# Kernel tuning notes

Measured on AMD Instinct MI355X. Metric: run time of the kernel, lower is better.

## Reference

```python
import jax, jax.numpy as jnp
import numpy as np

E = 8          # n_experts
K = 5          # n_active = int(0.7*E)
TEMP = float(np.e)

def _l2norm(v):
    n = jnp.linalg.norm(v, axis=-1, keepdims=True)
    return v / jnp.maximum(n, 1e-12)

def setup_inputs() -> dict:
    key = jax.random.key(0)
    ks = jax.random.split(key, 13)
    N, D, H, O = 4096, 2048, 4096, 2048
    s = lambda fan: 1.0 / np.sqrt(fan)
    return {
        "x":    jax.random.normal(ks[0], (N, D), jnp.float32),
        "Wg":   jax.random.normal(ks[1], (D, E), jnp.float32) * s(D),
        "bg":   jnp.zeros((E,), jnp.float32),
        "Wa":   jax.random.normal(ks[2], (D, 32), jnp.float32) * s(D),
        "ba":   jnp.zeros((32,), jnp.float32),
        "Wb":   jax.random.normal(ks[3], (32, 16), jnp.float32) * s(32),
        "bb":   jnp.zeros((16,), jnp.float32),
        "sigs": jax.random.normal(ks[4], (E, 16), jnp.float32) * 0.1,
        "W1":   jax.random.normal(ks[5], (E, D, H), jnp.float32) * s(D),
        "b1":   jnp.zeros((E, H), jnp.float32),
        "W2":   jax.random.normal(ks[6], (E, H, O), jnp.float32) * s(H),
        "b2":   jnp.zeros((E, O), jnp.float32),
    }

def reference(x, Wg, bg, Wa, ba, Wb, bb, sigs, W1, b1, W2, b2):
    # gating softmax (temperature = e)
    probs = jax.nn.softmax((x @ Wg + bg) / TEMP, axis=-1)          # [N, E]
    # PH feature match
    ph = jax.nn.relu(x @ Wa + ba) @ Wb + bb                        # [N, 16]
    ph_match = (_l2norm(ph) @ _l2norm(sigs).T + 1.0) / 2.0         # [N, E]
    effective = probs * ph_match                                   # [N, E]
    # top-k mask over experts
    _, idx = jax.lax.top_k(effective, K)                           # [N, K]
    mask = jnp.sum(jax.nn.one_hot(idx, E, dtype=effective.dtype), axis=-2)  # [N, E]
    weights = effective * mask
    weights = weights / (weights.sum(axis=-1, keepdims=True) + 1e-8)
    # dense all-expert FFN (eval mode: dropout is identity)
    h = jax.nn.relu(jnp.einsum('nd,edh->neh', x, W1) + b1)         # [N, E, H]
    outs = jnp.einsum('neh,eho->neo', h, W2) + b2                  # [N, E, O]
    return jnp.einsum('ne,neo->no', weights, outs)                 # [N, O]
```

## Files before the change

kernel.cpp:

```cpp
#include <hip/hip_runtime.h>
#include <hip/hip_bf16.h>
#include <stdint.h>

#define TOK  4096
#define DIM  2048
#define HID  4096
#define ODIM 2048
#define NEXP 8
#define KSEL 5
#define NSLOT (TOK * KSEL)

typedef __bf16 bf16x8 __attribute__((ext_vector_type(8)));
typedef float  f32x4  __attribute__((ext_vector_type(4)));
typedef unsigned short ushort8 __attribute__((ext_vector_type(8)));

__device__ __forceinline__ uint16_t f2bf(float f) {
  uint32_t u = __float_as_uint(f);
  u += 0x7FFFu + ((u >> 16) & 1u);
  return (uint16_t)(u >> 16);
}
__device__ __forceinline__ float bf2f(uint16_t h) {
  uint32_t u = ((uint32_t)h) << 16;
  return __uint_as_float(u);
}

#define GLD16(g, l) __builtin_amdgcn_global_load_lds(                      \
    (const __attribute__((address_space(1))) void*)(g),                    \
    (__attribute__((address_space(3))) void*)(l), 16, 0, 0)


__global__ void cast_x_kernel(const float* __restrict__ in,
                              uint16_t* __restrict__ out, int n4) {
  int i = blockIdx.x * blockDim.x + threadIdx.x;
  if (i >= n4) return;
  float4 v = ((const float4*)in)[i];
  ushort4 o;
  o.x = f2bf(v.x); o.y = f2bf(v.y); o.z = f2bf(v.z); o.w = f2bf(v.w);
  ((ushort4*)out)[i] = o;
}

__global__ void transpose_cast_kernel(const float* __restrict__ in,
                                      uint16_t* __restrict__ out,
                                      int R, int C, long inBatch, long outBatch) {
  __shared__ float tile[32][33];
  const float* src = in + (size_t)blockIdx.z * inBatch;
  uint16_t*    dst = out + (size_t)blockIdx.z * outBatch;
  int c0 = blockIdx.x * 32, r0 = blockIdx.y * 32;
  int tx = threadIdx.x, ty = threadIdx.y;
#pragma unroll
  for (int i = 0; i < 4; ++i)
    tile[ty + i * 8][tx] = src[(size_t)(r0 + ty + i * 8) * C + c0 + tx];
  __syncthreads();
#pragma unroll
  for (int i = 0; i < 4; ++i)
    dst[(size_t)(c0 + ty + i * 8) * R + r0 + tx] = f2bf(tile[tx][ty + i * 8]);
}


__global__ void routing_kernel(const float* __restrict__ x,
                               const float* __restrict__ Wg, const float* __restrict__ bg,
                               const float* __restrict__ Wa, const float* __restrict__ ba,
                               const float* __restrict__ Wb, const float* __restrict__ bb,
                               const float* __restrict__ sigs,
                               float* __restrict__ wts, int* __restrict__ selmask_g) {
  const int n    = blockIdx.x;
  const int lane = threadIdx.x;
  const float* xr = x + (size_t)n * DIM;

  float ga[NEXP]; float aa[32];
#pragma unroll
  for (int e = 0; e < NEXP; ++e) ga[e] = 0.f;
#pragma unroll
  for (int j = 0; j < 32; ++j) aa[j] = 0.f;

  for (int it = 0; it < DIM / 64; ++it) {
    int d = it * 64 + lane;
    float xv = xr[d];
    const float* wgr = Wg + (size_t)d * NEXP;
#pragma unroll
    for (int e = 0; e < NEXP; ++e) ga[e] += xv * wgr[e];
    const float* war = Wa + (size_t)d * 32;
#pragma unroll
    for (int j = 0; j < 32; ++j) aa[j] += xv * war[j];
  }
#pragma unroll
  for (int s = 1; s < 64; s <<= 1) {
#pragma unroll
    for (int e = 0; e < NEXP; ++e) ga[e] += __shfl_xor(ga[e], s);
#pragma unroll
    for (int j = 0; j < 32; ++j) aa[j] += __shfl_xor(aa[j], s);
  }

  float ph[16];
#pragma unroll
  for (int i = 0; i < 16; ++i) ph[i] = bb[i];
#pragma unroll
  for (int j = 0; j < 32; ++j) {
    float a = aa[j] + ba[j];
    a = a > 0.f ? a : 0.f;
#pragma unroll
    for (int i = 0; i < 16; ++i) ph[i] += a * Wb[j * 16 + i];
  }
  float nrm = 0.f;
#pragma unroll
  for (int i = 0; i < 16; ++i) nrm += ph[i] * ph[i];
  nrm = fmaxf(sqrtf(nrm), 1e-12f);

  const float invT = 0.36787944117144233f;
  float lg[NEXP], mx = -1e30f;
#pragma unroll
  for (int e = 0; e < NEXP; ++e) { lg[e] = (ga[e] + bg[e]) * invT; mx = fmaxf(mx, lg[e]); }
  float psum = 0.f, pr[NEXP];
#pragma unroll
  for (int e = 0; e < NEXP; ++e) { pr[e] = expf(lg[e] - mx); psum += pr[e]; }

  float eff[NEXP];
#pragma unroll
  for (int e = 0; e < NEXP; ++e) {
    const float* sg = sigs + e * 16;
    float dot = 0.f, sn = 0.f;
#pragma unroll
    for (int i = 0; i < 16; ++i) { dot += ph[i] * sg[i]; sn += sg[i] * sg[i]; }
    sn = fmaxf(sqrtf(sn), 1e-12f);
    float match = (dot / (nrm * sn) + 1.f) * 0.5f;
    eff[e] = (pr[e] / psum) * match;
  }

  int selmask = 0;
#pragma unroll
  for (int t = 0; t < KSEL; ++t) {
    int bi = 0; float bv = -1e30f;
#pragma unroll
    for (int e = 0; e < NEXP; ++e) {
      bool ok = !((selmask >> e) & 1);
      if (ok && eff[e] > bv) { bv = eff[e]; bi = e; }
    }
    selmask |= (1 << bi);
  }
  float wsum = 0.f, wv[NEXP];
#pragma unroll
  for (int e = 0; e < NEXP; ++e) {
    wv[e] = ((selmask >> e) & 1) ? eff[e] : 0.f;
    wsum += wv[e];
  }
  float inv = 1.f / (wsum + 1e-8f);
  if (lane == 0) {
#pragma unroll
    for (int e = 0; e < NEXP; ++e) wts[n * NEXP + e] = wv[e] * inv;
    selmask_g[n] = selmask;
  }
}


__global__ void listbuild_kernel(const int* __restrict__ selmask_g,
                                 const float* __restrict__ wts,
                                 int* __restrict__ cnt, int* __restrict__ base,
                                 int* __restrict__ list, int* __restrict__ slot_map,
                                 float* __restrict__ wrow) {
  const int e = blockIdx.x;
  const int t = threadIdx.x;
  __shared__ int cntT[256][NEXP];
  __shared__ int totAll[NEXP];
  __shared__ int sc[256];

  int msk[16];
  int c8[NEXP];
#pragma unroll
  for (int f = 0; f < NEXP; ++f) c8[f] = 0;
#pragma unroll
  for (int i = 0; i < 16; ++i) {
    msk[i] = selmask_g[t * 16 + i];
#pragma unroll
    for (int f = 0; f < NEXP; ++f) c8[f] += (msk[i] >> f) & 1;
  }
#pragma unroll
  for (int f = 0; f < NEXP; ++f) cntT[t][f] = c8[f];
  __syncthreads();

  if (t < NEXP) {
    int s = 0;
    for (int j = 0; j < 256; ++j) s += cntT[j][t];
    totAll[t] = s;
  }
  __syncthreads();

  if (e == 0 && t == 0) {
    int r = 0;
    for (int f = 0; f < NEXP; ++f) { cnt[f] = totAll[f]; base[f] = r; r += totAll[f]; }
  }
  int gbase = 0;
  for (int f = 0; f < e; ++f) gbase += totAll[f];

  sc[t] = c8[e];
  __syncthreads();
  for (int off = 1; off < 256; off <<= 1) {
    int v = (t >= off) ? sc[t - off] : 0;
    __syncthreads();
    sc[t] += v;
    __syncthreads();
  }
  int p = sc[t] - c8[e];

#pragma unroll
  for (int i = 0; i < 16; ++i) {
    const int n = t * 16 + i;
    const int m = msk[i];
    if ((m >> e) & 1) {
      list[e * TOK + p] = n;
      const int rank = __popc(m & ((1 << e) - 1));
      slot_map[n * KSEL + rank] = gbase + p;
      wrow[gbase + p] = wts[n * NEXP + e];
      ++p;
    }
  }
}


__global__ void gemm1_kernel(const uint16_t* __restrict__ xbf,
                             const uint16_t* __restrict__ W1T,
                             const int* __restrict__ cnt,
                             const int* __restrict__ base,
                             const int* __restrict__ list,
                             const float* __restrict__ wrow,
                             const float* __restrict__ b1,
                             uint16_t* __restrict__ hbuf) {
  __shared__ __attribute__((aligned(16))) uint16_t smA[128 * 64];
  __shared__ __attribute__((aligned(16))) uint16_t smB[128 * 64];
  const int e  = blockIdx.z;
  const int ce = cnt[e];
  const int tileM = blockIdx.y * 128;
  if (tileM >= ce) return;
  const int be    = base[e];
  const int tileN = blockIdx.x * 128;
  const int tid = threadIdx.x, lane = tid & 63, wid = tid >> 6;
  const int wr = wid >> 1, wc = wid & 1;
  const int* liste = list + e * TOK;

  const uint16_t* srcA[4]; const uint16_t* srcB[4]; uint32_t lof[4];
#pragma unroll
  for (int j = 0; j < 4; ++j) {
    const int f   = (wid * 4 + j) * 64 + lane;
    const int row = f >> 3;
    const int s8  = (f & 7) ^ (row & 7);
    int p = tileM + row; p = p < ce ? p : ce - 1;
    srcA[j] = xbf + (size_t)liste[p] * DIM + s8 * 8;
    srcB[j] = W1T + ((size_t)e * HID + tileN + row) * DIM + s8 * 8;
    lof[j]  = (wid * 4 + j) * 1024;
  }

  f32x4 acc[4][4];
#pragma unroll
  for (int m = 0; m < 4; ++m)
#pragma unroll
    for (int n = 0; n < 4; ++n) acc[m][n] = (f32x4){0.f, 0.f, 0.f, 0.f};

  for (int k0 = 0; k0 < DIM; k0 += 64) {
#pragma unroll
    for (int j = 0; j < 4; ++j) {
      GLD16(srcA[j] + k0, (char*)smA + lof[j]);
      GLD16(srcB[j] + k0, (char*)smB + lof[j]);
    }
    __syncthreads();
#pragma unroll
    for (int kk = 0; kk < 2; ++kk) {
      bf16x8 av[4], bv[4];
#pragma unroll
      for (int m = 0; m < 4; ++m) {
        const int row = wr * 64 + m * 16 + (lane & 15);
        const int g   = (kk * 4 + (lane >> 4)) ^ (row & 7);
        av[m] = *(const bf16x8*)(smA + row * 64 + g * 8);
      }
#pragma unroll
      for (int n = 0; n < 4; ++n) {
        const int row = wc * 64 + n * 16 + (lane & 15);
        const int g   = (kk * 4 + (lane >> 4)) ^ (row & 7);
        bv[n] = *(const bf16x8*)(smB + row * 64 + g * 8);
      }
#pragma unroll
      for (int m = 0; m < 4; ++m)
#pragma unroll
        for (int n = 0; n < 4; ++n)
          acc[m][n] = __builtin_amdgcn_mfma_f32_16x16x32_bf16(av[m], bv[n], acc[m][n], 0, 0, 0);
    }
    __syncthreads();
  }

  const float* b1e = b1 + (size_t)e * HID;
#pragma unroll
  for (int m = 0; m < 4; ++m)
#pragma unroll
    for (int r = 0; r < 4; ++r) {
      const int p = tileM + wr * 64 + m * 16 + ((lane >> 4) << 2) + r;
      if (p < ce) {
        const float w = wrow[be + p];
        uint16_t* orow = hbuf + (size_t)(be + p) * HID;
#pragma unroll
        for (int nf = 0; nf < 4; ++nf) {
          const int col = tileN + wc * 64 + nf * 16 + (lane & 15);
          float v = acc[m][nf][r] + b1e[col];
          v = v > 0.f ? v : 0.f;
          orow[col] = f2bf(v * w);
        }
      }
    }
}


__global__ void gemm2_kernel(const uint16_t* __restrict__ hbuf,
                             const uint16_t* __restrict__ W2T,
                             const int* __restrict__ cnt,
                             const int* __restrict__ base,
                             uint16_t* __restrict__ obuf) {
  __shared__ __attribute__((aligned(16))) uint16_t smA[128 * 64];
  __shared__ __attribute__((aligned(16))) uint16_t smB[128 * 64];
  const int e  = blockIdx.z;
  const int ce = cnt[e];
  const int tileM = blockIdx.y * 128;
  if (tileM >= ce) return;
  const int be    = base[e];
  const int tileN = blockIdx.x * 128;
  const int tid = threadIdx.x, lane = tid & 63, wid = tid >> 6;
  const int wr = wid >> 1, wc = wid & 1;

  const uint16_t* srcA[4]; const uint16_t* srcB[4]; uint32_t lof[4];
#pragma unroll
  for (int j = 0; j < 4; ++j) {
    const int f   = (wid * 4 + j) * 64 + lane;
    const int row = f >> 3;
    const int s8  = (f & 7) ^ (row & 7);
    srcA[j] = hbuf + (size_t)(be + tileM + row) * HID + s8 * 8;
    srcB[j] = W2T + (size_t)(tileN + row) * (NEXP * HID) + e * HID + s8 * 8;
    lof[j]  = (wid * 4 + j) * 1024;
  }

  f32x4 acc[4][4];
#pragma unroll
  for (int m = 0; m < 4; ++m)
#pragma unroll
    for (int n = 0; n < 4; ++n) acc[m][n] = (f32x4){0.f, 0.f, 0.f, 0.f};

  for (int k0 = 0; k0 < HID; k0 += 64) {
#pragma unroll
    for (int j = 0; j < 4; ++j) {
      GLD16(srcA[j] + k0, (char*)smA + lof[j]);
      GLD16(srcB[j] + k0, (char*)smB + lof[j]);
    }
    __syncthreads();
#pragma unroll
    for (int kk = 0; kk < 2; ++kk) {
      bf16x8 av[4], bv[4];
#pragma unroll
      for (int m = 0; m < 4; ++m) {
        const int row = wr * 64 + m * 16 + (lane & 15);
        const int g   = (kk * 4 + (lane >> 4)) ^ (row & 7);
        av[m] = *(const bf16x8*)(smA + row * 64 + g * 8);
      }
#pragma unroll
      for (int n = 0; n < 4; ++n) {
        const int row = wc * 64 + n * 16 + (lane & 15);
        const int g   = (kk * 4 + (lane >> 4)) ^ (row & 7);
        bv[n] = *(const bf16x8*)(smB + row * 64 + g * 8);
      }
#pragma unroll
      for (int m = 0; m < 4; ++m)
#pragma unroll
        for (int n = 0; n < 4; ++n)
          acc[m][n] = __builtin_amdgcn_mfma_f32_16x16x32_bf16(av[m], bv[n], acc[m][n], 0, 0, 0);
    }
    __syncthreads();
  }

#pragma unroll
  for (int m = 0; m < 4; ++m)
#pragma unroll
    for (int r = 0; r < 4; ++r) {
      const int p = tileM + wr * 64 + m * 16 + ((lane >> 4) << 2) + r;
      if (p < ce) {
        uint16_t* orow = obuf + (size_t)(be + p) * ODIM;
#pragma unroll
        for (int nf = 0; nf < 4; ++nf) {
          const int col = tileN + wc * 64 + nf * 16 + (lane & 15);
          orow[col] = f2bf(acc[m][nf][r]);
        }
      }
    }
}


__global__ void reduce_kernel(const uint16_t* __restrict__ obuf,
                              const int* __restrict__ slot_map,
                              const float* __restrict__ wts,
                              const float* __restrict__ b2,
                              float* __restrict__ out) {
  const int n = blockIdx.x;
  const int t = threadIdx.x;
  const int c = t * 8;

  int slots[KSEL];
#pragma unroll
  for (int k = 0; k < KSEL; ++k) slots[k] = slot_map[n * KSEL + k];
  float w8[NEXP];
#pragma unroll
  for (int e = 0; e < NEXP; ++e) w8[e] = wts[n * NEXP + e];

  float s[8];
#pragma unroll
  for (int j = 0; j < 8; ++j) s[j] = 0.f;
#pragma unroll
  for (int e = 0; e < NEXP; ++e) {
    const float4 b0 = *(const float4*)(b2 + (size_t)e * ODIM + c);
    const float4 b1v = *(const float4*)(b2 + (size_t)e * ODIM + c + 4);
    s[0] += w8[e] * b0.x; s[1] += w8[e] * b0.y; s[2] += w8[e] * b0.z; s[3] += w8[e] * b0.w;
    s[4] += w8[e] * b1v.x; s[5] += w8[e] * b1v.y; s[6] += w8[e] * b1v.z; s[7] += w8[e] * b1v.w;
  }
#pragma unroll
  for (int k = 0; k < KSEL; ++k) {
    const ushort8 v = *(const ushort8*)(obuf + (size_t)slots[k] * ODIM + c);
#pragma unroll
    for (int j = 0; j < 8; ++j) s[j] += bf2f(v[j]);
  }
  float4 o0 = make_float4(s[0], s[1], s[2], s[3]);
  float4 o1 = make_float4(s[4], s[5], s[6], s[7]);
  *(float4*)(out + (size_t)n * ODIM + c) = o0;
  *(float4*)(out + (size_t)n * ODIM + c + 4) = o1;
}


extern "C" void kernel_launch(void* const* d_in, const int* in_sizes, int n_in,
                              void* d_out, int out_size, void* d_ws, size_t ws_size,
                              hipStream_t stream) {
  const float* x    = (const float*)d_in[0];
  const float* Wg   = (const float*)d_in[1];
  const float* bg   = (const float*)d_in[2];
  const float* Wa   = (const float*)d_in[3];
  const float* ba   = (const float*)d_in[4];
  const float* Wb   = (const float*)d_in[5];
  const float* bb   = (const float*)d_in[6];
  const float* sigs = (const float*)d_in[7];
  const float* W1   = (const float*)d_in[8];
  const float* b1   = (const float*)d_in[9];
  const float* W2   = (const float*)d_in[10];
  const float* b2   = (const float*)d_in[11];
  float* out = (float*)d_out;

  char* ws = (char*)d_ws;
  float*    wts     = (float*)(ws + 0);
  int*      selmask = (int*)(ws + 131072);
  int*      cnt     = (int*)(ws + 147456);
  int*      base    = (int*)(ws + 147584);
  int*      slot_map= (int*)(ws + 151552);
  float*    wrow    = (float*)(ws + 233472);
  int*      list    = (int*)(ws + 315392);
  uint16_t* xbf     = (uint16_t*)(ws + 446464);
  uint16_t* W1T     = (uint16_t*)(ws + 17223680);
  uint16_t* W2T     = (uint16_t*)(ws + 151441408);
  uint16_t* hbuf    = (uint16_t*)(ws + 285659136);
  uint16_t* obuf    = (uint16_t*)(ws + 453431296);

  cast_x_kernel<<<(TOK * DIM / 4) / 256, 256, 0, stream>>>(x, xbf, TOK * DIM / 4);
  transpose_cast_kernel<<<dim3(HID / 32, DIM / 32, NEXP), dim3(32, 8), 0, stream>>>(
      W1, W1T, DIM, HID, (long)DIM * HID, (long)DIM * HID);
  transpose_cast_kernel<<<dim3(ODIM / 32, (NEXP * HID) / 32, 1), dim3(32, 8), 0, stream>>>(
      W2, W2T, NEXP * HID, ODIM, 0, 0);
  routing_kernel<<<TOK, 64, 0, stream>>>(x, Wg, bg, Wa, ba, Wb, bb, sigs, wts, selmask);
  listbuild_kernel<<<NEXP, 256, 0, stream>>>(selmask, wts, cnt, base, list, slot_map, wrow);

  gemm1_kernel<<<dim3(HID / 128, TOK / 128, NEXP), 256, 0, stream>>>(
      xbf, W1T, cnt, base, list, wrow, b1, hbuf);
  gemm2_kernel<<<dim3(ODIM / 128, TOK / 128, NEXP), 256, 0, stream>>>(
      hbuf, W2T, cnt, base, obuf);
  reduce_kernel<<<TOK, 256, 0, stream>>>(obuf, slot_map, wts, b2, out);
}
```

Before: 1.766 ms.

## Remap GEMM grids to 1D with expert-interleaved grouped tile order, per-expert W2T layout

Both grouped GEMMs now use a flattened 1D grid. The expert index is the fastest-varying dimension so consecutive workgroups spread across experts, and M/N tiles are grouped (8 M-tiles per N sweep in gemm1, 4 N-tiles per M sweep in gemm2) to improve L2 reuse of the A and B tiles. W2 is now transposed per expert into an [E, ODIM, HID] layout, so each expert's B rows are contiguous instead of strided by NEXP*HID. This aims to cut cache misses and DRAM traffic. The risk is that early-exiting empty tiles now sit interleaved across the dispatch order.

```diff
diff --git a/kernel.cpp b/kernel.cpp
--- a/kernel.cpp
+++ b/kernel.cpp
@@ -8,7 +8,6 @@
 #define ODIM 2048
 #define NEXP 8
 #define KSEL 5
-#define NSLOT (TOK * KSEL)
 
 typedef __bf16 bf16x8 __attribute__((ext_vector_type(8)));
 typedef float  f32x4  __attribute__((ext_vector_type(4)));
@@ -226,12 +225,19 @@
                              uint16_t* __restrict__ hbuf) {
   __shared__ __attribute__((aligned(16))) uint16_t smA[128 * 64];
   __shared__ __attribute__((aligned(16))) uint16_t smB[128 * 64];
-  const int e  = blockIdx.z;
+  const int d = blockIdx.x;
+  const int e = d & 7;
+  const int q = d >> 3;
+  const int grp = q >> 8;
+  const int rem = q & 255;
+  const int nt  = rem >> 3;
+  const int mt  = (grp << 3) | (rem & 7);
+
   const int ce = cnt[e];
-  const int tileM = blockIdx.y * 128;
+  const int tileM = mt * 128;
   if (tileM >= ce) return;
   const int be    = base[e];
-  const int tileN = blockIdx.x * 128;
+  const int tileN = nt * 128;
   const int tid = threadIdx.x, lane = tid & 63, wid = tid >> 6;
   const int wr = wid >> 1, wc = wid & 1;
   const int* liste = list + e * TOK;
@@ -313,12 +319,19 @@
                              uint16_t* __restrict__ obuf) {
   __shared__ __attribute__((aligned(16))) uint16_t smA[128 * 64];
   __shared__ __attribute__((aligned(16))) uint16_t smB[128 * 64];
-  const int e  = blockIdx.z;
+  const int d = blockIdx.x;
+  const int e = d & 7;
+  const int q = d >> 3;
+  const int grp = q >> 7;
+  const int rem = q & 127;
+  const int mt  = rem >> 2;
+  const int nt  = (grp << 2) | (rem & 3);
+
   const int ce = cnt[e];
-  const int tileM = blockIdx.y * 128;
+  const int tileM = mt * 128;
   if (tileM >= ce) return;
   const int be    = base[e];
-  const int tileN = blockIdx.x * 128;
+  const int tileN = nt * 128;
   const int tid = threadIdx.x, lane = tid & 63, wid = tid >> 6;
   const int wr = wid >> 1, wc = wid & 1;
 
@@ -329,7 +342,7 @@
     const int row = f >> 3;
     const int s8  = (f & 7) ^ (row & 7);
     srcA[j] = hbuf + (size_t)(be + tileM + row) * HID + s8 * 8;
-    srcB[j] = W2T + (size_t)(tileN + row) * (NEXP * HID) + e * HID + s8 * 8;
+    srcB[j] = W2T + ((size_t)e * ODIM + tileN + row) * HID + s8 * 8;
     lof[j]  = (wid * 4 + j) * 1024;
   }
 
@@ -460,14 +473,14 @@
   cast_x_kernel<<<(TOK * DIM / 4) / 256, 256, 0, stream>>>(x, xbf, TOK * DIM / 4);
   transpose_cast_kernel<<<dim3(HID / 32, DIM / 32, NEXP), dim3(32, 8), 0, stream>>>(
       W1, W1T, DIM, HID, (long)DIM * HID, (long)DIM * HID);
-  transpose_cast_kernel<<<dim3(ODIM / 32, (NEXP * HID) / 32, 1), dim3(32, 8), 0, stream>>>(
-      W2, W2T, NEXP * HID, ODIM, 0, 0);
+  transpose_cast_kernel<<<dim3(ODIM / 32, HID / 32, NEXP), dim3(32, 8), 0, stream>>>(
+      W2, W2T, HID, ODIM, (long)HID * ODIM, (long)ODIM * HID);
   routing_kernel<<<TOK, 64, 0, stream>>>(x, Wg, bg, Wa, ba, Wb, bb, sigs, wts, selmask);
   listbuild_kernel<<<NEXP, 256, 0, stream>>>(selmask, wts, cnt, base, list, slot_map, wrow);
 
-  gemm1_kernel<<<dim3(HID / 128, TOK / 128, NEXP), 256, 0, stream>>>(
+  gemm1_kernel<<<NEXP * 32 * 32, 256, 0, stream>>>(
       xbf, W1T, cnt, base, list, wrow, b1, hbuf);
-  gemm2_kernel<<<dim3(ODIM / 128, TOK / 128, NEXP), 256, 0, stream>>>(
+  gemm2_kernel<<<NEXP * 32 * 16, 256, 0, stream>>>(
       hbuf, W2T, cnt, base, obuf);
   reduce_kernel<<<TOK, 256, 0, stream>>>(obuf, slot_map, wts, b2, out);
 }
```

Measured after the change: 2.173 ms. +23.0%, slower.

## Replace both expert GEMMs with a 256x256 tile, 4-stage pipelined LDS kernel

Applied to the files above, without the earlier changes.

Both expert GEMMs now share one templated kernel that uses 256x256 output tiles with 512 threads and a 4-slot LDS ring buffer (K-step 32). Global-to-LDS loads are issued three stages ahead, with explicit vmcnt waits, split barriers and setprio around the MFMA bursts, so loads overlap with compute. The W2 transpose is also changed to a per-expert layout so both GEMMs index B the same way. The larger tiles improve operand reuse, but they add register pressure (128 accumulator floats per thread) and waste more work on partial M tiles at expert-count boundaries. The LDS layout also drops the XOR swizzle, which risks bank conflicts.

```diff
diff --git a/kernel.cpp b/kernel.cpp
--- a/kernel.cpp
+++ b/kernel.cpp
@@ -8,7 +8,6 @@
 #define ODIM 2048
 #define NEXP 8
 #define KSEL 5
-#define NSLOT (TOK * KSEL)
 
 typedef __bf16 bf16x8 __attribute__((ext_vector_type(8)));
 typedef float  f32x4  __attribute__((ext_vector_type(4)));
@@ -216,174 +215,144 @@
 }
 
 
-__global__ void gemm1_kernel(const uint16_t* __restrict__ xbf,
-                             const uint16_t* __restrict__ W1T,
-                             const int* __restrict__ cnt,
-                             const int* __restrict__ base,
-                             const int* __restrict__ list,
-                             const float* __restrict__ wrow,
-                             const float* __restrict__ b1,
-                             uint16_t* __restrict__ hbuf) {
-  __shared__ __attribute__((aligned(16))) uint16_t smA[128 * 64];
-  __shared__ __attribute__((aligned(16))) uint16_t smB[128 * 64];
+template <int MODE>
+__launch_bounds__(512, 2)
+__global__ void gemm_pipe_kernel(const uint16_t* __restrict__ A,
+                                 const uint16_t* __restrict__ Bt,
+                                 const int* __restrict__ cnt,
+                                 const int* __restrict__ base,
+                                 const int* __restrict__ list,
+                                 const float* __restrict__ wrow,
+                                 const float* __restrict__ bias,
+                                 uint16_t* __restrict__ outb,
+                                 int Kdim, int NTk, int Ncols) {
+  __shared__ __attribute__((aligned(16))) uint16_t lds[4 * 16384];
+
   const int e  = blockIdx.z;
   const int ce = cnt[e];
-  const int tileM = blockIdx.y * 128;
+  const int tileM = blockIdx.y * 256;
   if (tileM >= ce) return;
   const int be    = base[e];
-  const int tileN = blockIdx.x * 128;
+  const int tileN = blockIdx.x * 256;
   const int tid = threadIdx.x, lane = tid & 63, wid = tid >> 6;
-  const int wr = wid >> 1, wc = wid & 1;
-  const int* liste = list + e * TOK;
-
-  const uint16_t* srcA[4]; const uint16_t* srcB[4]; uint32_t lof[4];
-#pragma unroll
-  for (int j = 0; j < 4; ++j) {
-    const int f   = (wid * 4 + j) * 64 + lane;
-    const int row = f >> 3;
-    const int s8  = (f & 7) ^ (row & 7);
-    int p = tileM + row; p = p < ce ? p : ce - 1;
-    srcA[j] = xbf + (size_t)liste[p] * DIM + s8 * 8;
-    srcB[j] = W1T + ((size_t)e * HID + tileN + row) * DIM + s8 * 8;
-    lof[j]  = (wid * 4 + j) * 1024;
-  }
-
-  f32x4 acc[4][4];
-#pragma unroll
-  for (int m = 0; m < 4; ++m)
+  const int wr = wid >> 2, wc = wid & 3;
+  const int sr = (wid & 3) * 64 + lane;
+  const int sg = wid >> 2;
+
+  int pA = tileM + sr; pA = pA < ce ? pA : ce - 1;
+  const uint16_t* aRow;
+  if (MODE == 1) aRow = A + (size_t)list[e * TOK + pA] * Kdim;
+  else           aRow = A + (size_t)(be + pA) * Kdim;
+  const uint16_t* bRow = Bt + ((size_t)e * Ncols + tileN + sr) * Kdim;
+
+  char* lbase = (char*)lds + wid * 1024;
+
+#define STAGE_A(slotIdx, kOff)                                   \
+  { char* lb = lbase + (slotIdx) * 32768;                        \
+    GLD16(aRow + (kOff) + sg * 8,       lb);                     \
+    GLD16(aRow + (kOff) + (2 + sg) * 8, lb + 8192); }
+#define STAGE_B(slotIdx, kOff)                                   \
+  { char* lb = lbase + (slotIdx) * 32768 + 16384;                \
+    GLD16(bRow + (kOff) + sg * 8,       lb);                     \
+    GLD16(bRow + (kOff) + (2 + sg) * 8, lb + 8192); }
+
+  const int afrag = ((lane >> 4) << 8) + wr * 128 + (lane & 15);
+  const int bfrag = ((lane >> 4) << 8) + wc * 64 + (lane & 15);
+
+  f32x4 acc[8][4];
+#pragma unroll
+  for (int m = 0; m < 8; ++m)
 #pragma unroll
     for (int n = 0; n < 4; ++n) acc[m][n] = (f32x4){0.f, 0.f, 0.f, 0.f};
 
-  for (int k0 = 0; k0 < DIM; k0 += 64) {
-#pragma unroll
-    for (int j = 0; j < 4; ++j) {
-      GLD16(srcA[j] + k0, (char*)smA + lof[j]);
-      GLD16(srcB[j] + k0, (char*)smB + lof[j]);
-    }
-    __syncthreads();
-#pragma unroll
-    for (int kk = 0; kk < 2; ++kk) {
-      bf16x8 av[4], bv[4];
-#pragma unroll
-      for (int m = 0; m < 4; ++m) {
-        const int row = wr * 64 + m * 16 + (lane & 15);
-        const int g   = (kk * 4 + (lane >> 4)) ^ (row & 7);
-        av[m] = *(const bf16x8*)(smA + row * 64 + g * 8);
-      }
-#pragma unroll
-      for (int n = 0; n < 4; ++n) {
-        const int row = wc * 64 + n * 16 + (lane & 15);
-        const int g   = (kk * 4 + (lane >> 4)) ^ (row & 7);
-        bv[n] = *(const bf16x8*)(smB + row * 64 + g * 8);
-      }
-#pragma unroll
-      for (int m = 0; m < 4; ++m)
-#pragma unroll
-        for (int n = 0; n < 4; ++n)
-          acc[m][n] = __builtin_amdgcn_mfma_f32_16x16x32_bf16(av[m], bv[n], acc[m][n], 0, 0, 0);
-    }
-    __syncthreads();
-  }
-
-  const float* b1e = b1 + (size_t)e * HID;
-#pragma unroll
-  for (int m = 0; m < 4; ++m)
-#pragma unroll
-    for (int r = 0; r < 4; ++r) {
-      const int p = tileM + wr * 64 + m * 16 + ((lane >> 4) << 2) + r;
-      if (p < ce) {
-        const float w = wrow[be + p];
-        uint16_t* orow = hbuf + (size_t)(be + p) * HID;
-#pragma unroll
-        for (int nf = 0; nf < 4; ++nf) {
-          const int col = tileN + wc * 64 + nf * 16 + (lane & 15);
-          float v = acc[m][nf][r] + b1e[col];
-          v = v > 0.f ? v : 0.f;
-          orow[col] = f2bf(v * w);
+  STAGE_A(0, 0);  STAGE_B(0, 0);
+  STAGE_A(1, 32); STAGE_B(1, 32);
+  STAGE_A(2, 64); STAGE_B(2, 64);
+
+  for (int T = 0; T < NTk; ++T) {
+    if (T + 2 < NTk)      asm volatile("s_waitcnt vmcnt(8)" ::: "memory");
+    else if (T + 1 < NTk) asm volatile("s_waitcnt vmcnt(4)" ::: "memory");
+    else                  asm volatile("s_waitcnt vmcnt(0)" ::: "memory");
+    __builtin_amdgcn_sched_barrier(0);
+    __builtin_amdgcn_s_barrier();
+
+    const uint16_t* As = lds + (T & 3) * 16384;
+    const uint16_t* Bs = As + 8192;
+    const int kNext = (T + 3) * 32;
+    const bool doStage = (T + 3) < NTk;
+
+    bf16x8 av[8];
+#pragma unroll
+    for (int m = 0; m < 8; ++m)
+      av[m] = *(const bf16x8*)(As + (size_t)(afrag + m * 16) * 8);
+    bf16x8 bv0 = *(const bf16x8*)(Bs + (size_t)(bfrag + 0 * 16) * 8);
+    bf16x8 bv1 = *(const bf16x8*)(Bs + (size_t)(bfrag + 1 * 16) * 8);
+    if (doStage) STAGE_A((T + 3) & 3, kNext);
+    __builtin_amdgcn_s_barrier();
+    asm volatile("s_waitcnt lgkmcnt(0)" ::: "memory");
+    __builtin_amdgcn_sched_barrier(0);
+    __builtin_amdgcn_s_setprio(1);
+#pragma unroll
+    for (int m = 0; m < 8; ++m)
+      acc[m][0] = __builtin_amdgcn_mfma_f32_16x16x32_bf16(av[m], bv0, acc[m][0], 0, 0, 0);
+#pragma unroll
+    for (int m = 0; m < 8; ++m)
+      acc[m][1] = __builtin_amdgcn_mfma_f32_16x16x32_bf16(av[m], bv1, acc[m][1], 0, 0, 0);
+    __builtin_amdgcn_s_setprio(0);
+
+    bf16x8 bv2 = *(const bf16x8*)(Bs + (size_t)(bfrag + 2 * 16) * 8);
+    bf16x8 bv3 = *(const bf16x8*)(Bs + (size_t)(bfrag + 3 * 16) * 8);
+    if (doStage) STAGE_B((T + 3) & 3, kNext);
+    __builtin_amdgcn_s_barrier();
+    asm volatile("s_waitcnt lgkmcnt(0)" ::: "memory");
+    __builtin_amdgcn_sched_barrier(0);
+    __builtin_amdgcn_s_setprio(1);
+#pragma unroll
+    for (int m = 0; m < 8; ++m)
+      acc[m][2] = __builtin_amdgcn_mfma_f32_16x16x32_bf16(av[m], bv2, acc[m][2], 0, 0, 0);
+#pragma unroll
+    for (int m = 0; m < 8; ++m)
+      acc[m][3] = __builtin_amdgcn_mfma_f32_16x16x32_bf16(av[m], bv3, acc[m][3], 0, 0, 0);
+    __builtin_amdgcn_s_setprio(0);
+  }
+#undef STAGE_A
+#undef STAGE_B
+
+  if (MODE == 1) {
+    const float* b1e = bias + (size_t)e * Ncols;
+#pragma unroll
+    for (int m = 0; m < 8; ++m)
+#pragma unroll
+      for (int r = 0; r < 4; ++r) {
+        const int p = tileM + wr * 128 + m * 16 + ((lane >> 4) << 2) + r;
+        if (p < ce) {
+          const float w = wrow[be + p];
+          uint16_t* orow = outb + (size_t)(be + p) * Ncols;
+#pragma unroll
+          for (int n = 0; n < 4; ++n) {
+            const int col = tileN + wc * 64 + n * 16 + (lane & 15);
+            float v = acc[m][n][r] + b1e[col];
+            v = v > 0.f ? v : 0.f;
+            orow[col] = f2bf(v * w);
+          }
         }
       }
-    }
-}
-
-
-__global__ void gemm2_kernel(const uint16_t* __restrict__ hbuf,
-                             const uint16_t* __restrict__ W2T,
-                             const int* __restrict__ cnt,
-                             const int* __restrict__ base,
-                             uint16_t* __restrict__ obuf) {
-  __shared__ __attribute__((aligned(16))) uint16_t smA[128 * 64];
-  __shared__ __attribute__((aligned(16))) uint16_t smB[128 * 64];
-  const int e  = blockIdx.z;
-  const int ce = cnt[e];
-  const int tileM = blockIdx.y * 128;
-  if (tileM >= ce) return;
-  const int be    = base[e];
-  const int tileN = blockIdx.x * 128;
-  const int tid = threadIdx.x, lane = tid & 63, wid = tid >> 6;
-  const int wr = wid >> 1, wc = wid & 1;
-
-  const uint16_t* srcA[4]; const uint16_t* srcB[4]; uint32_t lof[4];
-#pragma unroll
-  for (int j = 0; j < 4; ++j) {
-    const int f   = (wid * 4 + j) * 64 + lane;
-    const int row = f >> 3;
-    const int s8  = (f & 7) ^ (row & 7);
-    srcA[j] = hbuf + (size_t)(be + tileM + row) * HID + s8 * 8;
-    srcB[j] = W2T + (size_t)(tileN + row) * (NEXP * HID) + e * HID + s8 * 8;
-    lof[j]  = (wid * 4 + j) * 1024;
-  }
-
-  f32x4 acc[4][4];
-#pragma unroll
-  for (int m = 0; m < 4; ++m)
-#pragma unroll
-    for (int n = 0; n < 4; ++n) acc[m][n] = (f32x4){0.f, 0.f, 0.f, 0.f};
-
-  for (int k0 = 0; k0 < HID; k0 += 64) {
-#pragma unroll
-    for (int j = 0; j < 4; ++j) {
-      GLD16(srcA[j] + k0, (char*)smA + lof[j]);
-      GLD16(srcB[j] + k0, (char*)smB + lof[j]);
-    }
-    __syncthreads();
-#pragma unroll
-    for (int kk = 0; kk < 2; ++kk) {
-      bf16x8 av[4], bv[4];
-#pragma unroll
-      for (int m = 0; m < 4; ++m) {
-        const int row = wr * 64 + m * 16 + (lane & 15);
-        const int g   = (kk * 4 + (lane >> 4)) ^ (row & 7);
-        av[m] = *(const bf16x8*)(smA + row * 64 + g * 8);
-      }
-#pragma unroll
-      for (int n = 0; n < 4; ++n) {
-        const int row = wc * 64 + n * 16 + (lane & 15);
-        const int g   = (kk * 4 + (lane >> 4)) ^ (row & 7);
-        bv[n] = *(const bf16x8*)(smB + row * 64 + g * 8);
-      }
-#pragma unroll
-      for (int m = 0; m < 4; ++m)
-#pragma unroll
-        for (int n = 0; n < 4; ++n)
-          acc[m][n] = __builtin_amdgcn_mfma_f32_16x16x32_bf16(av[m], bv[n], acc[m][n], 0, 0, 0);
-    }
-    __syncthreads();
-  }
-
-#pragma unroll
-  for (int m = 0; m < 4; ++m)
-#pragma unroll
-    for (int r = 0; r < 4; ++r) {
-      const int p = tileM + wr * 64 + m * 16 + ((lane >> 4) << 2) + r;
-      if (p < ce) {
-        uint16_t* orow = obuf + (size_t)(be + p) * ODIM;
-#pragma unroll
-        for (int nf = 0; nf < 4; ++nf) {
-          const int col = tileN + wc * 64 + nf * 16 + (lane & 15);
-          orow[col] = f2bf(acc[m][nf][r]);
+  } else {
+#pragma unroll
+    for (int m = 0; m < 8; ++m)
+#pragma unroll
+      for (int r = 0; r < 4; ++r) {
+        const int p = tileM + wr * 128 + m * 16 + ((lane >> 4) << 2) + r;
+        if (p < ce) {
+          uint16_t* orow = outb + (size_t)(be + p) * Ncols;
+#pragma unroll
+          for (int n = 0; n < 4; ++n) {
+            const int col = tileN + wc * 64 + n * 16 + (lane & 15);
+            orow[col] = f2bf(acc[m][n][r]);
+          }
         }
       }
-    }
+  }
 }
 
 
@@ -460,14 +429,14 @@
   cast_x_kernel<<<(TOK * DIM / 4) / 256, 256, 0, stream>>>(x, xbf, TOK * DIM / 4);
   transpose_cast_kernel<<<dim3(HID / 32, DIM / 32, NEXP), dim3(32, 8), 0, stream>>>(
       W1, W1T, DIM, HID, (long)DIM * HID, (long)DIM * HID);
-  transpose_cast_kernel<<<dim3(ODIM / 32, (NEXP * HID) / 32, 1), dim3(32, 8), 0, stream>>>(
-      W2, W2T, NEXP * HID, ODIM, 0, 0);
+  transpose_cast_kernel<<<dim3(ODIM / 32, HID / 32, NEXP), dim3(32, 8), 0, stream>>>(
+      W2, W2T, HID, ODIM, (long)HID * ODIM, (long)ODIM * HID);
   routing_kernel<<<TOK, 64, 0, stream>>>(x, Wg, bg, Wa, ba, Wb, bb, sigs, wts, selmask);
   listbuild_kernel<<<NEXP, 256, 0, stream>>>(selmask, wts, cnt, base, list, slot_map, wrow);
 
-  gemm1_kernel<<<dim3(HID / 128, TOK / 128, NEXP), 256, 0, stream>>>(
-      xbf, W1T, cnt, base, list, wrow, b1, hbuf);
-  gemm2_kernel<<<dim3(ODIM / 128, TOK / 128, NEXP), 256, 0, stream>>>(
-      hbuf, W2T, cnt, base, obuf);
+  gemm_pipe_kernel<1><<<dim3(HID / 256, 16, NEXP), 512, 0, stream>>>(
+      xbf, W1T, cnt, base, list, wrow, b1, hbuf, DIM, DIM / 32, HID);
+  gemm_pipe_kernel<2><<<dim3(ODIM / 256, 16, NEXP), 512, 0, stream>>>(
+      hbuf, W2T, cnt, base, nullptr, nullptr, nullptr, obuf, HID, HID / 32, ODIM);
   reduce_kernel<<<TOK, 256, 0, stream>>>(obuf, slot_map, wts, b2, out);
 }
```

Measured after the change: 1.529 ms. -13.4%, faster.
